# Kernel tuning notes

Hardware: AMD Instinct MI355X
Metric: run time of the kernel (lower is better)

The kernel has to match this reference:

```python
import jax, jax.numpy as jnp
import numpy as np

N = 50000
C = 128        # ch_in == hidden_dim (required by gather/BatchNorm in original)
HD = 128
HEADS = 4
INNER = HD * HEADS
TOPK = 5
EPS = 1e-5


def setup_inputs() -> dict:
    key = jax.random.key(0)
    ks = jax.random.split(key, 12)
    g = lambda k, shape, s: (jax.random.normal(k, shape, jnp.float32) * s)
    return {
        'h_f': g(ks[0], (N, C), 1.0),
        'x_f': g(ks[1], (N, C), 1.0),
        'x_c': g(ks[2], (N, 3), 1.0),
        'h_c': g(ks[3], (N, 3), 1.0),
        'Wq': g(ks[4], (C, INNER), 0.05),
        'Wk': g(ks[5], (C, INNER), 0.05),
        'Wv': g(ks[6], (C, INNER), 0.05),
        'Wo': g(ks[7], (INNER, C), 0.05),
        'bo': jnp.zeros((C,), jnp.float32),
        'gamma_a': jnp.ones((C,), jnp.float32),
        'beta_a': jnp.zeros((C,), jnp.float32),
        'Wp': g(ks[8], (C, C), 0.05),
        'bp': jnp.zeros((C,), jnp.float32),
        'gamma_p': jnp.ones((C,), jnp.float32),
        'beta_p': jnp.zeros((C,), jnp.float32),
    }


def batchnorm(x, gamma, beta):
    # training-mode BatchNorm1d: batch statistics (biased variance)
    mu = jnp.mean(x, axis=0)
    var = jnp.mean((x - mu) ** 2, axis=0)
    return gamma * (x - mu) * jax.lax.rsqrt(var + EPS) + beta


def atten(h, x, Wq, Wk, Wv, Wo, bo, gamma, beta):
    # h: [n, K, C], x: [n, C]
    n, K, c = h.shape
    q = (x @ Wq).reshape(n, HEADS, HD)          # [n, h, d]
    k = (h @ Wk).reshape(n, K, HEADS, HD)       # [n, K, h, d]
    v = (h @ Wv).reshape(n, K, HEADS, HD)       # [n, K, h, d]
    w = jnp.einsum('nkhd,nhd->nhk', k, q)[..., None] * (c ** -0.5)  # [n,h,K,1]
    # faithful to original: softmax over a size-1 trailing axis (-> all ones)
    w = jax.nn.softmax(w, axis=-1)[..., 0]       # [n, h, K]
    out = jnp.einsum('nkhd,nhk->nhd', v, w).reshape(n, INNER)
    out = out @ Wo + bo
    return jax.nn.relu(batchnorm(out, gamma, beta))


def getnewpoints(x_f, h_f, x_c, h_c, Wq, Wk, Wv, Wo, bo, gamma, beta):
    n = x_f.shape[0]
    if n < TOPK:
        return x_f
    sim = x_c @ h_c.T                            # [n, n]
    # torch.topk(sim, TOPK, dim=0).indices -> [TOPK, n]; lax.top_k works on last axis
    tidx = jax.lax.top_k(sim.T, TOPK)[1]         # [n, TOPK] == torch indices.T
    # faithful flatten order of the original: [TOPK, n] row-major -> reshape [n, TOPK]
    neigh = tidx.T.reshape(-1).reshape(n, TOPK)  # [n, TOPK]
    hn = h_f[neigh]                              # gather: [n, TOPK, C]
    hcat = jnp.concatenate([hn, x_f[:, None, :]], axis=1)  # [n, TOPK+1, C]
    return atten(hcat, x_f, Wq, Wk, Wv, Wo, bo, gamma, beta)


def reference(h_f, x_f, x_c, h_c, Wq, Wk, Wv, Wo, bo, gamma_a, beta_a,
              Wp, bp, gamma_p, beta_p):
    n = x_f.shape[0]
    f = int(2 * n ** (2.0 / 3.0))                # fenkuai, static
    m = n // f
    at = (Wq, Wk, Wv, Wo, bo, gamma_a, beta_a)

    def chunk(args):
        xf, hf, xc, hc = args
        return getnewpoints(xf, hf, xc, hc, *at)

    full = jax.lax.map(chunk, (
        x_f[:m * f].reshape(m, f, -1),
        h_f[:m * f].reshape(m, f, -1),
        x_c[:m * f].reshape(m, f, 3),
        h_c[:m * f].reshape(m, f, 3),
    ))                                            # [m, f, C]
    rem = getnewpoints(x_f[m * f:], h_f[m * f:], x_c[m * f:], h_c[m * f:], *at)
    result = jnp.concatenate([full.reshape(-1, x_f.shape[1]), rem], axis=0)
    # point_transforms_h: Linear -> BatchNorm1d -> ReLU
    result = result @ Wp + bp
    return jax.nn.relu(batchnorm(result, gamma_p, beta_p))
```

## Files before the change

kernel.cpp:

```cpp
#include <hip/hip_runtime.h>
#include <hip/hip_bf16.h>
#include <math.h>

#define NTOT    50000
#define CDIM    128
#define FCHUNK  2714
#define MCH     18
#define NREM    (NTOT - MCH*FCHUNK)
#define NCHUNKS 19
#define TOPKN   5
#define INNERD  512
#define BNEPS   1e-5f
#define SEGS    64
#define RPT     8
#define CAP     25
#define APAD    136
#define WPAD    40

typedef __attribute__((ext_vector_type(8))) short short8v;
typedef __attribute__((ext_vector_type(4))) float float4v;

static __device__ __forceinline__ int chunk_n(int chunk) {
    return (chunk < MCH) ? FCHUNK : NREM;
}

static __device__ __forceinline__ unsigned short bf16hi(float v) {
    return (unsigned short)(__float_as_uint(v) >> 16);
}

#define INS5(s, jj, V0,V1,V2,V3,V4,I0,I1,I2,I3,I4) \
    if (s > V4) { \
        if (s > V0)      { V4=V3;I4=I3; V3=V2;I3=I2; V2=V1;I2=I1; V1=V0;I1=I0; V0=s;I0=jj; } \
        else if (s > V1) { V4=V3;I4=I3; V3=V2;I3=I2; V2=V1;I2=I1; V1=s;I1=jj; } \
        else if (s > V2) { V4=V3;I4=I3; V3=V2;I3=I2; V2=s;I2=jj; } \
        else if (s > V3) { V4=V3;I4=I3; V3=s;I3=jj; } \
        else             { V4=s;I4=jj; } \
    }

#define INS5C(s, jj, V0,V1,V2,V3,V4,I0,I1,I2,I3,I4) \
    if ((s > V4) || (s == V4 && jj < I4)) { \
        if ((s > V0) || (s == V0 && jj < I0))      { V4=V3;I4=I3; V3=V2;I3=I2; V2=V1;I2=I1; V1=V0;I1=I0; V0=s;I0=jj; } \
        else if ((s > V1) || (s == V1 && jj < I1)) { V4=V3;I4=I3; V3=V2;I3=I2; V2=V1;I2=I1; V1=s;I1=jj; } \
        else if ((s > V2) || (s == V2 && jj < I2)) { V4=V3;I4=I3; V3=V2;I3=I2; V2=s;I2=jj; } \
        else if ((s > V3) || (s == V3 && jj < I3)) { V4=V3;I4=I3; V3=s;I3=jj; } \
        else                                        { V4=s;I4=jj; } \
    }

#define CAS(x, y) { float lo_ = fminf(x, y), hi_ = fmaxf(x, y); x = lo_; y = hi_; }

__global__ void k1_w1(const float* __restrict__ Wv, const float* __restrict__ Wo,
                      unsigned short* __restrict__ Th)
{
    __shared__ float s_wv[INNERD];
    int r = blockIdx.x;
    for (int t = threadIdx.x; t < INNERD; t += blockDim.x) s_wv[t] = Wv[r*INNERD + t];
    __syncthreads();
    int c = threadIdx.x;
    float acc = 0.f;
    #pragma unroll 8
    for (int k = 0; k < INNERD; ++k) acc = fmaf(s_wv[k], Wo[k*CDIM + c], acc);
    Th[c*CDIM + r] = bf16hi(acc);
}

__global__ void k1b_wp(const float* __restrict__ Wp, unsigned short* __restrict__ Th)
{
    int r = blockIdx.x, c = threadIdx.x;
    Th[c*CDIM + r] = bf16hi(Wp[r*CDIM + c]);
}

__global__ __launch_bounds__(512) void k2_topk(const float* __restrict__ x_c,
                                               const float* __restrict__ h_c,
                                               int* __restrict__ tidx)
{
    __shared__ float2 s_x01[FCHUNK];
    __shared__ float  s_x2[FCHUNK];
    __shared__ float  scratch[4224];
    int chunk = blockIdx.y;
    int base  = chunk * FCHUNK;
    int n     = chunk_n(chunk);
    int row0  = blockIdx.x * 64;
    if (row0 >= n) return;

    for (int e = threadIdx.x; e < n; e += 512) {
        s_x01[e] = make_float2(x_c[(base+e)*3], x_c[(base+e)*3 + 1]);
        s_x2[e]  = x_c[(base+e)*3 + 2];
    }
    __syncthreads();

    int seg = threadIdx.x & 63;
    int g   = threadIdx.x >> 6;

    float h0[RPT], h1[RPT], h2[RPT];
    #pragma unroll
    for (int r = 0; r < RPT; ++r) {
        int row = row0 + g + 8*r;
        bool v = row < n;
        h0[r] = v ? h_c[(base+row)*3  ] : 0.f;
        h1[r] = v ? h_c[(base+row)*3+1] : 0.f;
        h2[r] = v ? h_c[(base+row)*3+2] : 0.f;
    }

    float m[RPT];
    #pragma unroll
    for (int r = 0; r < RPT; ++r) m[r] = -INFINITY;
    #pragma unroll 2
    for (int j = seg; j < n; j += SEGS) {
        float2 x01 = s_x01[j];
        float  xz  = s_x2[j];
        #pragma unroll
        for (int r = 0; r < RPT; ++r)
            m[r] = fmaxf(m[r], fmaf(xz,h2[r], fmaf(x01.y,h1[r], x01.x*h0[r])));
    }
    float* s_segmax = scratch;
    float* s_thr    = scratch + 64*65;
    #pragma unroll
    for (int r = 0; r < RPT; ++r) s_segmax[(g+8*r)*65 + seg] = m[r];
    __syncthreads();

    if (threadIdx.x < 64) {
        int lr = threadIdx.x;
        const float* sm = &s_segmax[lr*65];
        float b[8];
        #pragma unroll
        for (int ss = 0; ss < 8; ++ss) {
            float m0 = fmaxf(fmaxf(sm[ss*8+0],sm[ss*8+1]), fmaxf(sm[ss*8+2],sm[ss*8+3]));
            float m1 = fmaxf(fmaxf(sm[ss*8+4],sm[ss*8+5]), fmaxf(sm[ss*8+6],sm[ss*8+7]));
            b[ss] = fmaxf(m0, m1);
        }
        float b0=b[0],b1=b[1],b2=b[2],b3=b[3],b4=b[4],b5=b[5],b6=b[6],b7=b[7];
        CAS(b0,b1); CAS(b2,b3); CAS(b4,b5); CAS(b6,b7);
        CAS(b0,b2); CAS(b1,b3); CAS(b4,b6); CAS(b5,b7);
        CAS(b1,b2); CAS(b5,b6);
        CAS(b0,b4); CAS(b1,b5); CAS(b2,b6); CAS(b3,b7);
        CAS(b2,b4); CAS(b3,b5);
        CAS(b1,b2); CAS(b3,b4); CAS(b5,b6);
        s_thr[lr] = (row0 + lr < n) ? b3 : INFINITY;
    }
    __syncthreads();
    float thr[RPT];
    #pragma unroll
    for (int r = 0; r < RPT; ++r) thr[r] = s_thr[g + 8*r];
    __syncthreads();

    int*   s_cnt = (int*)scratch;
    float* s_cv  = scratch + 64;
    int*   s_cj  = (int*)(scratch + 64 + 64*CAP);
    if (threadIdx.x < 64) s_cnt[threadIdx.x] = 0;
    __syncthreads();

    #pragma unroll 2
    for (int j = seg; j < n; j += SEGS) {
        float2 x01 = s_x01[j];
        float  xz  = s_x2[j];
        #pragma unroll
        for (int r = 0; r < RPT; ++r) {
            float d = fmaf(xz,h2[r], fmaf(x01.y,h1[r], x01.x*h0[r]));
            if (!(d < thr[r])) {
                int lr = g + 8*r;
                int p = atomicAdd(&s_cnt[lr], 1);
                if (p < CAP) { s_cv[lr*CAP+p] = d; s_cj[lr*CAP+p] = j; }
            }
        }
    }
    __syncthreads();

    if (threadIdx.x < 64) {
        int lr = threadIdx.x, row = row0 + lr;
        if (row < n) {
            float v0=-INFINITY,v1=-INFINITY,v2=-INFINITY,v3=-INFINITY,v4=-INFINITY;
            int i0=0x7fffffff,i1=0x7fffffff,i2=0x7fffffff,i3=0x7fffffff,i4=0x7fffffff;
            int mcnt = s_cnt[lr];
            if (mcnt <= CAP) {
                for (int t = 0; t < mcnt; ++t) {
                    float s = s_cv[lr*CAP + t]; int jj = s_cj[lr*CAP + t];
                    INS5C(s, jj, v0,v1,v2,v3,v4, i0,i1,i2,i3,i4);
                }
            } else {
                float ha = h_c[(base+row)*3], hb = h_c[(base+row)*3+1], hc2 = h_c[(base+row)*3+2];
                v0=v1=v2=v3=v4=-INFINITY; i0=i1=i2=i3=i4=0;
                for (int jj = 0; jj < n; ++jj) {
                    float s = fmaf(s_x2[jj],hc2, fmaf(s_x01[jj].y,hb, s_x01[jj].x*ha));
                    INS5(s, jj, v0,v1,v2,v3,v4, i0,i1,i2,i3,i4);
                }
            }
            int o = (base+row)*TOPKN;
            tidx[o+0]=i0; tidx[o+1]=i1; tidx[o+2]=i2; tidx[o+3]=i3; tidx[o+4]=i4;
        }
    }
}

__global__ __launch_bounds__(256) void k3_gemm1(const float* __restrict__ x_f,
                         const float* __restrict__ h_f,
                         const int* __restrict__ tidx,
                         const unsigned short* __restrict__ Th,
                         const float* __restrict__ bo, float* __restrict__ A,
                         float* __restrict__ cstats)
{
    __shared__ unsigned short s_ah[64][APAD];
    __shared__ unsigned short s_wh[128][WPAD];
    __shared__ int s_nb[64][TOPKN];
    __shared__ float s_red[256];
    int chunk = blockIdx.y;
    int base  = chunk * FCHUNK;
    int n     = chunk_n(chunk);
    int row0  = blockIdx.x * 64;
    if (row0 >= n) return;

    for (int e = threadIdx.x; e < 64*TOPKN; e += 256) {
        int r = e / TOPKN, k = e % TOPKN;
        int il = row0 + r;
        int nb = 0;
        if (il < n) {
            int p = il*TOPKN + k;
            int q, m;
            if (n == FCHUNK) { q = p / FCHUNK; m = p - q*FCHUNK; }
            else             { q = p / NREM;   m = p - q*NREM; }
            nb = tidx[(base + m)*TOPKN + q];
        }
        s_nb[r][k] = nb;
    }
    __syncthreads();

    for (int e = threadIdx.x; e < 64*32; e += 256) {
        int r = e >> 5, c4 = e & 31;
        float4 acc4 = make_float4(0.f,0.f,0.f,0.f);
        int gr = row0 + r;
        if (gr < n) {
            acc4 = *(const float4*)&x_f[(base+gr)*CDIM + c4*4];
            #pragma unroll
            for (int k = 0; k < TOPKN; ++k) {
                float4 h4 = *(const float4*)&h_f[(base + s_nb[r][k])*CDIM + c4*4];
                acc4.x += h4.x; acc4.y += h4.y; acc4.z += h4.z; acc4.w += h4.w;
            }
        }
        uint2 ph;
        ph.x = (unsigned)bf16hi(acc4.x) | ((unsigned)bf16hi(acc4.y) << 16);
        ph.y = (unsigned)bf16hi(acc4.z) | ((unsigned)bf16hi(acc4.w) << 16);
        *(uint2*)&s_ah[r][c4*4] = ph;
    }

    int lane = threadIdx.x & 63;
    int w    = threadIdx.x >> 6;
    int lr   = lane & 15, lg = lane >> 4;
    float4v acc[8];
    #pragma unroll
    for (int ct = 0; ct < 8; ++ct) acc[ct] = (float4v){0.f,0.f,0.f,0.f};

    for (int ks = 0; ks < 4; ++ks) {
        __syncthreads();
        {
            int col = threadIdx.x >> 1, half = threadIdx.x & 1;
            const uint4* gh = (const uint4*)&Th[col*CDIM + ks*32 + half*16];
            uint4* dh = (uint4*)&s_wh[col][half*16];
            dh[0] = gh[0]; dh[1] = gh[1];
        }
        __syncthreads();
        short8v a_h = *(const short8v*)&s_ah[w*16 + lr][ks*32 + lg*8];
        #pragma unroll
        for (int ct = 0; ct < 8; ++ct) {
            short8v b_h = *(const short8v*)&s_wh[ct*16 + lr][lg*8];
            acc[ct] = __builtin_amdgcn_mfma_f32_16x16x32_bf16(a_h, b_h, acc[ct], 0,0,0);
        }
    }

    float ps[8], ps2[8];
    #pragma unroll
    for (int ct = 0; ct < 8; ++ct) { ps[ct] = 0.f; ps2[ct] = 0.f; }
    #pragma unroll
    for (int ct = 0; ct < 8; ++ct) {
        int gcol = ct*16 + lr;
        float b = bo[gcol];
        #pragma unroll
        for (int ri = 0; ri < 4; ++ri) {
            int grow = row0 + w*16 + lg*4 + ri;
            if (grow < n) {
                float v = acc[ct][ri] + b;
                A[(base+grow)*CDIM + gcol] = v;
                ps[ct] += v; ps2[ct] = fmaf(v, v, ps2[ct]);
            }
        }
    }
    #pragma unroll
    for (int ct = 0; ct < 8; ++ct) {
        ps[ct]  += __shfl_xor(ps[ct], 16, 64);  ps[ct]  += __shfl_xor(ps[ct], 32, 64);
        ps2[ct] += __shfl_xor(ps2[ct], 16, 64); ps2[ct] += __shfl_xor(ps2[ct], 32, 64);
    }
    __syncthreads();
    s_red[threadIdx.x] = 0.f;
    __syncthreads();
    if (lane < 16) {
        #pragma unroll
        for (int ct = 0; ct < 8; ++ct) {
            int gcol = ct*16 + lane;
            atomicAdd(&s_red[gcol*2],   ps[ct]);
            atomicAdd(&s_red[gcol*2+1], ps2[ct]);
        }
    }
    __syncthreads();
    if (threadIdx.x < 128) {
        atomicAdd(&cstats[chunk*256 + threadIdx.x],       s_red[threadIdx.x*2]);
        atomicAdd(&cstats[chunk*256 + 128 + threadIdx.x], s_red[threadIdx.x*2+1]);
    }
}

__global__ __launch_bounds__(256) void k5_gemm2(const float* __restrict__ A,
                         const unsigned short* __restrict__ Th,
                         const float* __restrict__ bp, const float* __restrict__ gamma_a,
                         const float* __restrict__ beta_a, const float* __restrict__ cstats,
                         float* __restrict__ Z, float* __restrict__ gstats)
{
    __shared__ unsigned short s_ah[64][APAD];
    __shared__ unsigned short s_wh[128][WPAD];
    __shared__ float s_sc[CDIM], s_sf[CDIM];
    __shared__ float s_red[256];
    int chunk = blockIdx.y;
    int base  = chunk * FCHUNK;
    int n     = chunk_n(chunk);
    int row0  = blockIdx.x * 64;
    if (row0 >= n) return;

    if (threadIdx.x < CDIM) {
        int c = threadIdx.x;
        float inv_n = 1.f / (float)n;
        float mu  = cstats[chunk*256 + c] * inv_n;
        float var = cstats[chunk*256 + 128 + c] * inv_n - mu*mu;
        float sc  = gamma_a[c] * rsqrtf(var + BNEPS);
        s_sc[c] = sc;
        s_sf[c] = beta_a[c] - mu*sc;
    }
    __syncthreads();

    for (int e = threadIdx.x; e < 64*32; e += 256) {
        int r = e >> 5, c4 = e & 31;
        float4 y = make_float4(0.f,0.f,0.f,0.f);
        int gr = row0 + r;
        if (gr < n) {
            float4 a4 = *(const float4*)&A[(base+gr)*CDIM + c4*4];
            int c = c4*4;
            y.x = fmaxf(fmaf(a4.x, s_sc[c+0], s_sf[c+0]), 0.f);
            y.y = fmaxf(fmaf(a4.y, s_sc[c+1], s_sf[c+1]), 0.f);
            y.z = fmaxf(fmaf(a4.z, s_sc[c+2], s_sf[c+2]), 0.f);
            y.w = fmaxf(fmaf(a4.w, s_sc[c+3], s_sf[c+3]), 0.f);
        }
        uint2 ph;
        ph.x = (unsigned)bf16hi(y.x) | ((unsigned)bf16hi(y.y) << 16);
        ph.y = (unsigned)bf16hi(y.z) | ((unsigned)bf16hi(y.w) << 16);
        *(uint2*)&s_ah[r][c4*4] = ph;
    }

    int lane = threadIdx.x & 63;
    int w    = threadIdx.x >> 6;
    int lr   = lane & 15, lg = lane >> 4;
    float4v acc[8];
    #pragma unroll
    for (int ct = 0; ct < 8; ++ct) acc[ct] = (float4v){0.f,0.f,0.f,0.f};

    for (int ks = 0; ks < 4; ++ks) {
        __syncthreads();
        {
            int col = threadIdx.x >> 1, half = threadIdx.x & 1;
            const uint4* gh = (const uint4*)&Th[col*CDIM + ks*32 + half*16];
            uint4* dh = (uint4*)&s_wh[col][half*16];
            dh[0] = gh[0]; dh[1] = gh[1];
        }
        __syncthreads();
        short8v a_h = *(const short8v*)&s_ah[w*16 + lr][ks*32 + lg*8];
        #pragma unroll
        for (int ct = 0; ct < 8; ++ct) {
            short8v b_h = *(const short8v*)&s_wh[ct*16 + lr][lg*8];
            acc[ct] = __builtin_amdgcn_mfma_f32_16x16x32_bf16(a_h, b_h, acc[ct], 0,0,0);
        }
    }

    float ps[8], ps2[8];
    #pragma unroll
    for (int ct = 0; ct < 8; ++ct) { ps[ct] = 0.f; ps2[ct] = 0.f; }
    #pragma unroll
    for (int ct = 0; ct < 8; ++ct) {
        int gcol = ct*16 + lr;
        float b = bp[gcol];
        #pragma unroll
        for (int ri = 0; ri < 4; ++ri) {
            int grow = row0 + w*16 + lg*4 + ri;
            if (grow < n) {
                float v = acc[ct][ri] + b;
                Z[(base+grow)*CDIM + gcol] = v;
                ps[ct] += v; ps2[ct] = fmaf(v, v, ps2[ct]);
            }
        }
    }
    #pragma unroll
    for (int ct = 0; ct < 8; ++ct) {
        ps[ct]  += __shfl_xor(ps[ct], 16, 64);  ps[ct]  += __shfl_xor(ps[ct], 32, 64);
        ps2[ct] += __shfl_xor(ps2[ct], 16, 64); ps2[ct] += __shfl_xor(ps2[ct], 32, 64);
    }
    __syncthreads();
    s_red[threadIdx.x] = 0.f;
    __syncthreads();
    if (lane < 16) {
        #pragma unroll
        for (int ct = 0; ct < 8; ++ct) {
            int gcol = ct*16 + lane;
            atomicAdd(&s_red[gcol*2],   ps[ct]);
            atomicAdd(&s_red[gcol*2+1], ps2[ct]);
        }
    }
    __syncthreads();
    if (threadIdx.x < 128) {
        atomicAdd(&gstats[threadIdx.x],       s_red[threadIdx.x*2]);
        atomicAdd(&gstats[128 + threadIdx.x], s_red[threadIdx.x*2+1]);
    }
}

__global__ void k7_final(float* __restrict__ Z, const float* __restrict__ gstats,
                         const float* __restrict__ gamma_p, const float* __restrict__ beta_p)
{
    __shared__ float s_sc[CDIM], s_sf[CDIM];
    if (threadIdx.x < CDIM) {
        int c = threadIdx.x;
        const float inv_n = 1.f / (float)NTOT;
        float mu  = gstats[c] * inv_n;
        float var = gstats[128 + c] * inv_n - mu*mu;
        float sc  = gamma_p[c] * rsqrtf(var + BNEPS);
        s_sc[c] = sc;
        s_sf[c] = beta_p[c] - mu*sc;
    }
    __syncthreads();
    int i4 = blockIdx.x * blockDim.x + threadIdx.x;
    if (i4 >= NTOT*32) return;
    float4 z = ((const float4*)Z)[i4];
    int c = (i4 & 31) * 4;
    z.x = fmaxf(fmaf(z.x, s_sc[c+0], s_sf[c+0]), 0.f);
    z.y = fmaxf(fmaf(z.y, s_sc[c+1], s_sf[c+1]), 0.f);
    z.z = fmaxf(fmaf(z.z, s_sc[c+2], s_sf[c+2]), 0.f);
    z.w = fmaxf(fmaf(z.w, s_sc[c+3], s_sf[c+3]), 0.f);
    ((float4*)Z)[i4] = z;
}

extern "C" void kernel_launch(void* const* d_in, const int* in_sizes, int n_in,
                              void* d_out, int out_size, void* d_ws, size_t ws_size,
                              hipStream_t stream)
{
    (void)in_sizes; (void)n_in; (void)out_size; (void)ws_size;
    const float* h_f  = (const float*)d_in[0];
    const float* x_f  = (const float*)d_in[1];
    const float* x_c  = (const float*)d_in[2];
    const float* h_c  = (const float*)d_in[3];
    const float* Wv   = (const float*)d_in[6];
    const float* Wo   = (const float*)d_in[7];
    const float* bo   = (const float*)d_in[8];
    const float* ga   = (const float*)d_in[9];
    const float* ba   = (const float*)d_in[10];
    const float* Wp   = (const float*)d_in[11];
    const float* bp   = (const float*)d_in[12];
    const float* gp   = (const float*)d_in[13];
    const float* betp = (const float*)d_in[14];

    char*  ws     = (char*)d_ws;
    unsigned short* Th = (unsigned short*)ws;
    float* cstats = (float*)(ws + 65536);
    float* gstats = (float*)(ws + 65536 + 19456);
    int*   tidx   = (int*)(ws + 65536 + 20480);
    float* A      = (float*)(ws + 65536 + 20480 + 1000000);
    float* Z      = (float*)d_out;

    hipMemsetAsync(ws + 65536, 0, 20480, stream);

    k1_w1    <<<dim3(CDIM),        dim3(CDIM), 0, stream>>>(Wv, Wo, Th);
    k2_topk  <<<dim3(43, NCHUNKS), dim3(512),  0, stream>>>(x_c, h_c, tidx);
    k3_gemm1 <<<dim3(43, NCHUNKS), dim3(256),  0, stream>>>(x_f, h_f, tidx, Th, bo, A, cstats);
    k1b_wp   <<<dim3(CDIM),        dim3(CDIM), 0, stream>>>(Wp, Th);
    k5_gemm2 <<<dim3(43, NCHUNKS), dim3(256),  0, stream>>>(A, Th, bp, ga, ba, cstats, Z, gstats);
    k7_final <<<dim3((NTOT*32 + 255)/256), dim3(256), 0, stream>>>(Z, gstats, gp, betp);
}
```

Before: 154.1 us.

## Store attention output as bf16 and split GEMM tiles across eight waves

```diff
diff --git a/kernel.cpp b/kernel.cpp
--- a/kernel.cpp
+++ b/kernel.cpp
@@ -28,6 +28,10 @@
     return (unsigned short)(__float_as_uint(v) >> 16);
 }
 
+static __device__ __forceinline__ float bf16tof(unsigned short u) {
+    return __uint_as_float((unsigned)u << 16);
+}
+
 #define INS5(s, jj, V0,V1,V2,V3,V4,I0,I1,I2,I3,I4) \
     if (s > V4) { \
         if (s > V0)      { V4=V3;I4=I3; V3=V2;I3=I2; V2=V1;I2=I1; V1=V0;I1=I0; V0=s;I0=jj; } \
@@ -62,10 +66,10 @@
     Th[c*CDIM + r] = bf16hi(acc);
 }
 
-__global__ void k1b_wp(const float* __restrict__ Wp, unsigned short* __restrict__ Th)
+__global__ void k1b_wp(const float* __restrict__ Wp, unsigned short* __restrict__ Thp)
 {
     int r = blockIdx.x, c = threadIdx.x;
-    Th[c*CDIM + r] = bf16hi(Wp[r*CDIM + c]);
+    Thp[c*CDIM + r] = bf16hi(Wp[r*CDIM + c]);
 }
 
 __global__ __launch_bounds__(512) void k2_topk(const float* __restrict__ x_c,
@@ -189,11 +193,11 @@
     }
 }
 
-__global__ __launch_bounds__(256) void k3_gemm1(const float* __restrict__ x_f,
+__global__ __launch_bounds__(512) void k3_gemm1(const float* __restrict__ x_f,
                          const float* __restrict__ h_f,
                          const int* __restrict__ tidx,
                          const unsigned short* __restrict__ Th,
-                         const float* __restrict__ bo, float* __restrict__ A,
+                         const float* __restrict__ bo, unsigned short* __restrict__ A,
                          float* __restrict__ cstats)
 {
     __shared__ unsigned short s_ah[64][APAD];
@@ -206,7 +210,8 @@
     int row0  = blockIdx.x * 64;
     if (row0 >= n) return;
 
-    for (int e = threadIdx.x; e < 64*TOPKN; e += 256) {
+    if (threadIdx.x < 64*TOPKN) {
+        int e = threadIdx.x;
         int r = e / TOPKN, k = e % TOPKN;
         int il = row0 + r;
         int nb = 0;
@@ -221,7 +226,7 @@
     }
     __syncthreads();
 
-    for (int e = threadIdx.x; e < 64*32; e += 256) {
+    for (int e = threadIdx.x; e < 64*32; e += 512) {
         int r = e >> 5, c4 = e & 31;
         float4 acc4 = make_float4(0.f,0.f,0.f,0.f);
         int gr = row0 + r;
@@ -241,57 +246,57 @@
 
     int lane = threadIdx.x & 63;
     int w    = threadIdx.x >> 6;
+    int wr   = w & 3;
+    int wc   = w >> 2;
     int lr   = lane & 15, lg = lane >> 4;
-    float4v acc[8];
-    #pragma unroll
-    for (int ct = 0; ct < 8; ++ct) acc[ct] = (float4v){0.f,0.f,0.f,0.f};
+    float4v acc[4];
+    #pragma unroll
+    for (int ct = 0; ct < 4; ++ct) acc[ct] = (float4v){0.f,0.f,0.f,0.f};
 
     for (int ks = 0; ks < 4; ++ks) {
         __syncthreads();
         {
-            int col = threadIdx.x >> 1, half = threadIdx.x & 1;
-            const uint4* gh = (const uint4*)&Th[col*CDIM + ks*32 + half*16];
-            uint4* dh = (uint4*)&s_wh[col][half*16];
-            dh[0] = gh[0]; dh[1] = gh[1];
+            int col = threadIdx.x >> 2, q = threadIdx.x & 3;
+            *(uint4*)&s_wh[col][q*8] = *(const uint4*)&Th[col*CDIM + ks*32 + q*8];
         }
         __syncthreads();
-        short8v a_h = *(const short8v*)&s_ah[w*16 + lr][ks*32 + lg*8];
-        #pragma unroll
-        for (int ct = 0; ct < 8; ++ct) {
-            short8v b_h = *(const short8v*)&s_wh[ct*16 + lr][lg*8];
+        short8v a_h = *(const short8v*)&s_ah[wr*16 + lr][ks*32 + lg*8];
+        #pragma unroll
+        for (int ct = 0; ct < 4; ++ct) {
+            short8v b_h = *(const short8v*)&s_wh[(wc*4 + ct)*16 + lr][lg*8];
             acc[ct] = __builtin_amdgcn_mfma_f32_16x16x32_bf16(a_h, b_h, acc[ct], 0,0,0);
         }
     }
 
-    float ps[8], ps2[8];
-    #pragma unroll
-    for (int ct = 0; ct < 8; ++ct) { ps[ct] = 0.f; ps2[ct] = 0.f; }
-    #pragma unroll
-    for (int ct = 0; ct < 8; ++ct) {
-        int gcol = ct*16 + lr;
+    float ps[4], ps2[4];
+    #pragma unroll
+    for (int ct = 0; ct < 4; ++ct) { ps[ct] = 0.f; ps2[ct] = 0.f; }
+    #pragma unroll
+    for (int ct = 0; ct < 4; ++ct) {
+        int gcol = (wc*4 + ct)*16 + lr;
         float b = bo[gcol];
         #pragma unroll
         for (int ri = 0; ri < 4; ++ri) {
-            int grow = row0 + w*16 + lg*4 + ri;
+            int grow = row0 + wr*16 + lg*4 + ri;
             if (grow < n) {
                 float v = acc[ct][ri] + b;
-                A[(base+grow)*CDIM + gcol] = v;
+                A[(base+grow)*CDIM + gcol] = bf16hi(v);
                 ps[ct] += v; ps2[ct] = fmaf(v, v, ps2[ct]);
             }
         }
     }
     #pragma unroll
-    for (int ct = 0; ct < 8; ++ct) {
+    for (int ct = 0; ct < 4; ++ct) {
         ps[ct]  += __shfl_xor(ps[ct], 16, 64);  ps[ct]  += __shfl_xor(ps[ct], 32, 64);
         ps2[ct] += __shfl_xor(ps2[ct], 16, 64); ps2[ct] += __shfl_xor(ps2[ct], 32, 64);
     }
     __syncthreads();
-    s_red[threadIdx.x] = 0.f;
+    if (threadIdx.x < 256) s_red[threadIdx.x] = 0.f;
     __syncthreads();
     if (lane < 16) {
         #pragma unroll
-        for (int ct = 0; ct < 8; ++ct) {
-            int gcol = ct*16 + lane;
+        for (int ct = 0; ct < 4; ++ct) {
+            int gcol = (wc*4 + ct)*16 + lane;
             atomicAdd(&s_red[gcol*2],   ps[ct]);
             atomicAdd(&s_red[gcol*2+1], ps2[ct]);
         }
@@ -303,8 +308,8 @@
     }
 }
 
-__global__ __launch_bounds__(256) void k5_gemm2(const float* __restrict__ A,
-                         const unsigned short* __restrict__ Th,
+__global__ __launch_bounds__(512) void k5_gemm2(const unsigned short* __restrict__ A,
+                         const unsigned short* __restrict__ Thp,
                          const float* __restrict__ bp, const float* __restrict__ gamma_a,
                          const float* __restrict__ beta_a, const float* __restrict__ cstats,
                          float* __restrict__ Z, float* __restrict__ gstats)
@@ -330,58 +335,61 @@
     }
     __syncthreads();
 
-    for (int e = threadIdx.x; e < 64*32; e += 256) {
+    for (int e = threadIdx.x; e < 64*32; e += 512) {
         int r = e >> 5, c4 = e & 31;
-        float4 y = make_float4(0.f,0.f,0.f,0.f);
+        uint2 ph = make_uint2(0u, 0u);
         int gr = row0 + r;
         if (gr < n) {
-            float4 a4 = *(const float4*)&A[(base+gr)*CDIM + c4*4];
+            uint2 a2 = *(const uint2*)&A[(base+gr)*CDIM + c4*4];
             int c = c4*4;
-            y.x = fmaxf(fmaf(a4.x, s_sc[c+0], s_sf[c+0]), 0.f);
-            y.y = fmaxf(fmaf(a4.y, s_sc[c+1], s_sf[c+1]), 0.f);
-            y.z = fmaxf(fmaf(a4.z, s_sc[c+2], s_sf[c+2]), 0.f);
-            y.w = fmaxf(fmaf(a4.w, s_sc[c+3], s_sf[c+3]), 0.f);
-        }
-        uint2 ph;
-        ph.x = (unsigned)bf16hi(y.x) | ((unsigned)bf16hi(y.y) << 16);
-        ph.y = (unsigned)bf16hi(y.z) | ((unsigned)bf16hi(y.w) << 16);
+            float a0 = bf16tof((unsigned short)(a2.x & 0xFFFF));
+            float a1 = bf16tof((unsigned short)(a2.x >> 16));
+            float a2f = bf16tof((unsigned short)(a2.y & 0xFFFF));
+            float a3 = bf16tof((unsigned short)(a2.y >> 16));
+            float y0 = fmaxf(fmaf(a0, s_sc[c+0], s_sf[c+0]), 0.f);
+            float y1 = fmaxf(fmaf(a1, s_sc[c+1], s_sf[c+1]), 0.f);
+            float y2 = fmaxf(fmaf(a2f, s_sc[c+2], s_sf[c+2]), 0.f);
+            float y3 = fmaxf(fmaf(a3, s_sc[c+3], s_sf[c+3]), 0.f);
+            ph.x = (unsigned)bf16hi(y0) | ((unsigned)bf16hi(y1) << 16);
+            ph.y = (unsigned)bf16hi(y2) | ((unsigned)bf16hi(y3) << 16);
+        }
         *(uint2*)&s_ah[r][c4*4] = ph;
     }
 
     int lane = threadIdx.x & 63;
     int w    = threadIdx.x >> 6;
+    int wr   = w & 3;
+    int wc   = w >> 2;
     int lr   = lane & 15, lg = lane >> 4;
-    float4v acc[8];
-    #pragma unroll
-    for (int ct = 0; ct < 8; ++ct) acc[ct] = (float4v){0.f,0.f,0.f,0.f};
+    float4v acc[4];
+    #pragma unroll
+    for (int ct = 0; ct < 4; ++ct) acc[ct] = (float4v){0.f,0.f,0.f,0.f};
 
     for (int ks = 0; ks < 4; ++ks) {
         __syncthreads();
         {
-            int col = threadIdx.x >> 1, half = threadIdx.x & 1;
-            const uint4* gh = (const uint4*)&Th[col*CDIM + ks*32 + half*16];
-            uint4* dh = (uint4*)&s_wh[col][half*16];
-            dh[0] = gh[0]; dh[1] = gh[1];
+            int col = threadIdx.x >> 2, q = threadIdx.x & 3;
+            *(uint4*)&s_wh[col][q*8] = *(const uint4*)&Thp[col*CDIM + ks*32 + q*8];
         }
         __syncthreads();
-        short8v a_h = *(const short8v*)&s_ah[w*16 + lr][ks*32 + lg*8];
-        #pragma unroll
-        for (int ct = 0; ct < 8; ++ct) {
-            short8v b_h = *(const short8v*)&s_wh[ct*16 + lr][lg*8];
+        short8v a_h = *(const short8v*)&s_ah[wr*16 + lr][ks*32 + lg*8];
+        #pragma unroll
+        for (int ct = 0; ct < 4; ++ct) {
+            short8v b_h = *(const short8v*)&s_wh[(wc*4 + ct)*16 + lr][lg*8];
             acc[ct] = __builtin_amdgcn_mfma_f32_16x16x32_bf16(a_h, b_h, acc[ct], 0,0,0);
         }
     }
 
-    float ps[8], ps2[8];
-    #pragma unroll
-    for (int ct = 0; ct < 8; ++ct) { ps[ct] = 0.f; ps2[ct] = 0.f; }
-    #pragma unroll
-    for (int ct = 0; ct < 8; ++ct) {
-        int gcol = ct*16 + lr;
+    float ps[4], ps2[4];
+    #pragma unroll
+    for (int ct = 0; ct < 4; ++ct) { ps[ct] = 0.f; ps2[ct] = 0.f; }
+    #pragma unroll
+    for (int ct = 0; ct < 4; ++ct) {
+        int gcol = (wc*4 + ct)*16 + lr;
         float b = bp[gcol];
         #pragma unroll
         for (int ri = 0; ri < 4; ++ri) {
-            int grow = row0 + w*16 + lg*4 + ri;
+            int grow = row0 + wr*16 + lg*4 + ri;
             if (grow < n) {
                 float v = acc[ct][ri] + b;
                 Z[(base+grow)*CDIM + gcol] = v;
@@ -390,17 +398,17 @@
         }
     }
     #pragma unroll
-    for (int ct = 0; ct < 8; ++ct) {
+    for (int ct = 0; ct < 4; ++ct) {
         ps[ct]  += __shfl_xor(ps[ct], 16, 64);  ps[ct]  += __shfl_xor(ps[ct], 32, 64);
         ps2[ct] += __shfl_xor(ps2[ct], 16, 64); ps2[ct] += __shfl_xor(ps2[ct], 32, 64);
     }
     __syncthreads();
-    s_red[threadIdx.x] = 0.f;
+    if (threadIdx.x < 256) s_red[threadIdx.x] = 0.f;
     __syncthreads();
     if (lane < 16) {
         #pragma unroll
-        for (int ct = 0; ct < 8; ++ct) {
-            int gcol = ct*16 + lane;
+        for (int ct = 0; ct < 4; ++ct) {
+            int gcol = (wc*4 + ct)*16 + lane;
             atomicAdd(&s_red[gcol*2],   ps[ct]);
             atomicAdd(&s_red[gcol*2+1], ps2[ct]);
         }
@@ -457,19 +465,20 @@
     const float* betp = (const float*)d_in[14];
 
     char*  ws     = (char*)d_ws;
-    unsigned short* Th = (unsigned short*)ws;
+    unsigned short* Th  = (unsigned short*)ws;
+    unsigned short* Thp = (unsigned short*)(ws + 32768);
     float* cstats = (float*)(ws + 65536);
     float* gstats = (float*)(ws + 65536 + 19456);
     int*   tidx   = (int*)(ws + 65536 + 20480);
-    float* A      = (float*)(ws + 65536 + 20480 + 1000000);
+    unsigned short* A = (unsigned short*)(ws + 65536 + 20480 + 1000000);
     float* Z      = (float*)d_out;
 
     hipMemsetAsync(ws + 65536, 0, 20480, stream);
 
     k1_w1    <<<dim3(CDIM),        dim3(CDIM), 0, stream>>>(Wv, Wo, Th);
+    k1b_wp   <<<dim3(CDIM),        dim3(CDIM), 0, stream>>>(Wp, Thp);
     k2_topk  <<<dim3(43, NCHUNKS), dim3(512),  0, stream>>>(x_c, h_c, tidx);
-    k3_gemm1 <<<dim3(43, NCHUNKS), dim3(256),  0, stream>>>(x_f, h_f, tidx, Th, bo, A, cstats);
-    k1b_wp   <<<dim3(CDIM),        dim3(CDIM), 0, stream>>>(Wp, Th);
-    k5_gemm2 <<<dim3(43, NCHUNKS), dim3(256),  0, stream>>>(A, Th, bp, ga, ba, cstats, Z, gstats);
+    k3_gemm1 <<<dim3(43, NCHUNKS), dim3(512),  0, stream>>>(x_f, h_f, tidx, Th, bo, A, cstats);
+    k5_gemm2 <<<dim3(43, NCHUNKS), dim3(512),  0, stream>>>(A, Thp, bp, ga, ba, cstats, Z, gstats);
     k7_final <<<dim3((NTOT*32 + 255)/256), dim3(256), 0, stream>>>(Z, gstats, gp, betp);
 }
```

Result: faster. 149.3 us (median of 2 runs) (-3.1%).
